# Kernel optimization log

Hardware: AMD Instinct MI355X
Metric: run time of the kernel (lower is better)

## Reference

```python
import jax, jax.numpy as jnp
import numpy as np

N, E, H, K, C, NMOD = 50000, 600000, 128, 5, 60, 12  # nodes, edges, hidden, hops, classes, 6 blocks * 2 modules


def setup_inputs() -> dict:
    key = jax.random.key(0)
    ks = iter(jax.random.split(key, 48))
    def rn(shape, scale=0.05):
        return jax.random.normal(next(ks), shape, jnp.float32) * scale
    return {
        "node_features": rn((N, 2), 1.0),
        "lap_pe": rn((N, K), 1.0),
        "edge_feat": rn((E, 4), 1.0),
        "src": jax.random.randint(next(ks), (E,), 0, N),
        "dst": jax.random.randint(next(ks), (E,), 0, N),
        "in_w": rn((2, H)), "in_b": jnp.zeros((H,), jnp.float32),
        "pos_w": rn((K, H)), "pos_b": jnp.zeros((H,), jnp.float32),
        "edge_w": rn((4, H)), "edge_b": jnp.zeros((H,), jnp.float32),
        "conv_w": rn((NMOD, 2, (K + 1) * H, H)), "conv_b": jnp.zeros((NMOD, 2, H), jnp.float32),
        "bn_g": jnp.ones((NMOD, 2, H), jnp.float32), "bn_b": jnp.zeros((NMOD, 2, H), jnp.float32),
        "ff_w": rn((NMOD, H, H)), "ff_b": jnp.zeros((NMOD, H), jnp.float32),
        "pose_w1": rn((H, H)), "pose_b1": jnp.zeros((H,), jnp.float32),
        "pose_w2": rn((H, 3)), "pose_b2": jnp.zeros((3,), jnp.float32),
        "lab_w1": rn((H, H)), "lab_b1": jnp.zeros((H,), jnp.float32),
        "lab_w2": rn((H, C)), "lab_b2": jnp.zeros((C,), jnp.float32),
    }


def _bn(x, g, b):
    # BatchNorm1d in training mode: stats over node axis
    m = x.mean(0)
    v = x.var(0)
    return (x - m) * jax.lax.rsqrt(v + 1e-5) * g + b


def reference(node_features, lap_pe, edge_feat, src, dst,
              in_w, in_b, pos_w, pos_b, edge_w, edge_b,
              conv_w, conv_b, bn_g, bn_b, ff_w, ff_b,
              pose_w1, pose_b1, pose_w2, pose_b2,
              lab_w1, lab_b1, lab_w2, lab_b2):
    seg = jax.ops.segment_sum
    # symmetric degree norm (in-degree, clamped to 1) as in DGL TAGConv
    deg = seg(jnp.ones((E,), node_features.dtype), dst, num_segments=N)
    norm = jnp.clip(deg, 1.0) ** -0.5  # [N]

    # edge feature aggregation: copy_e -> sum onto dst
    agg_e = seg(edge_feat @ edge_w + edge_b, dst, num_segments=N)  # [N,H]
    h = node_features @ in_w + in_b + lap_pe @ pos_w + pos_b + agg_e

    def tagconv(x, W, b):
        # fstack = [x, Ax, ..., A^K x] with A = D^-1/2 A D^-1/2, then single linear
        fs = [x]
        for _ in range(K):
            z = fs[-1] * norm[:, None]
            z = seg(z[src], dst, num_segments=N) * norm[:, None]
            fs.append(z)
        return jnp.concatenate(fs, axis=-1) @ W + b  # [N,H]

    for m in range(NMOD):  # 6 blocks x 2 TAGConvModules, sequential
        h_in = h
        h = jax.nn.relu(_bn(tagconv(h, conv_w[m, 0], conv_b[m, 0]), bn_g[m, 0], bn_b[m, 0]))
        h = jax.nn.relu(_bn(tagconv(h, conv_w[m, 1], conv_b[m, 1]), bn_g[m, 1], bn_b[m, 1]))
        h = h @ ff_w[m] + ff_b[m] + h_in  # dropout = identity (eval)

    pose = jax.nn.relu(h @ pose_w1 + pose_b1) @ pose_w2 + pose_b2  # [N,3]
    y = h.mean(0)  # dgl.mean_nodes (single batched graph)
    labels = jax.nn.relu(y @ lab_w1 + lab_b1) @ lab_w2 + lab_b2  # [C]
    return pose, labels
```

## Files before the change

kernel.cpp:

```cpp
#include <hip/hip_runtime.h>

#define NN 50000
#define EE 600000
#define HH 128
#define KK 5
#define CC 60
#define NMODS 12

typedef _Float16 f16;
typedef __attribute__((ext_vector_type(8))) _Float16 f16x8;
typedef __attribute__((ext_vector_type(4))) _Float16 f16x4;
typedef __attribute__((ext_vector_type(16))) float f32x16;

#define GLOBAL_AS __attribute__((address_space(1)))
#define LDS_AS __attribute__((address_space(3)))


__global__ void k_deg(const int* __restrict__ dst, int* __restrict__ deg) {
    int i = blockIdx.x * 256 + threadIdx.x;
    if (i < EE) atomicAdd(&deg[dst[i]], 1);
}

__global__ __launch_bounds__(1024) void k_scan(const int* __restrict__ deg, int* __restrict__ rs) {
    __shared__ int sm[1024];
    __shared__ int carry;
    int tid = threadIdx.x;
    if (tid == 0) carry = 0;
    __syncthreads();
    for (int base = 0; base < NN; base += 1024) {
        int i = base + tid;
        int v = (i < NN) ? deg[i] : 0;
        sm[tid] = v;
        __syncthreads();
        for (int off = 1; off < 1024; off <<= 1) {
            int t = (tid >= off) ? sm[tid - off] : 0;
            __syncthreads();
            sm[tid] += t;
            __syncthreads();
        }
        int incl = sm[tid];
        int c = carry;
        if (i < NN) rs[i] = c + incl - v;
        __syncthreads();
        if (tid == 1023) carry = c + incl;
        __syncthreads();
    }
    if (tid == 0) rs[NN] = carry;
}

__global__ void k_norm(const int* __restrict__ deg, float* __restrict__ norm) {
    int i = blockIdx.x * 256 + threadIdx.x;
    if (i < NN) {
        int d = deg[i];
        float fd = (float)(d < 1 ? 1 : d);
        norm[i] = 1.0f / sqrtf(fd);
    }
}

__global__ void k_fill(const int* __restrict__ src, const int* __restrict__ dst,
                       const int* __restrict__ rs, int* __restrict__ cursor,
                       int* __restrict__ csrc, int* __restrict__ ceid) {
    int i = blockIdx.x * 256 + threadIdx.x;
    if (i >= EE) return;
    int d = dst[i];
    int slot = atomicAdd(&cursor[d], 1);
    int p = rs[d] + slot;
    csrc[p] = src[i];
    ceid[p] = i;
}


__global__ void k_cvtw(const float* __restrict__ conv_w, const float* __restrict__ ff_w,
                       const float* __restrict__ pose_w1,
                       f16* __restrict__ wc, f16* __restrict__ wf, f16* __restrict__ wp) {
    int i = blockIdx.x * 256 + threadIdx.x;
    const int NCW = 24 * 128 * 768;
    const int NFW = 12 * 128 * 128;
    const int NPW = 128 * 128;
    if (i < NCW) {
        int mat = i / (128 * 768); int rem = i - mat * (128 * 768);
        int col = rem / 768; int k = rem - col * 768;
        wc[i] = (f16)conv_w[(size_t)mat * 768 * 128 + (size_t)k * 128 + col];
    } else if (i < NCW + NFW) {
        int j = i - NCW;
        int mat = j / (128 * 128); int rem = j - mat * (128 * 128);
        int col = rem / 128; int k = rem - col * 128;
        wf[j] = (f16)ff_w[(size_t)mat * 128 * 128 + k * 128 + col];
    } else if (i < NCW + NFW + NPW) {
        int j = i - NCW - NFW;
        int col = j / 128; int k = j - col * 128;
        wp[j] = (f16)pose_w1[k * 128 + col];
    }
}


__global__ __launch_bounds__(128) void k_h0(
    const float* __restrict__ nf, const float* __restrict__ pe, const float* __restrict__ ef,
    const int* __restrict__ rs, const int* __restrict__ ceid,
    const float* __restrict__ in_w, const float* __restrict__ in_b,
    const float* __restrict__ pos_w, const float* __restrict__ pos_b,
    const float* __restrict__ edge_w, const float* __restrict__ edge_b,
    float* __restrict__ h, f16* __restrict__ zc) {
    int n = blockIdx.x;
    int f = threadIdx.x;
    float v = in_b[f] + pos_b[f];
    v += nf[n * 2 + 0] * in_w[f] + nf[n * 2 + 1] * in_w[HH + f];
#pragma unroll
    for (int k = 0; k < KK; k++) v += pe[n * KK + k] * pos_w[k * HH + f];
    float e0 = edge_w[f], e1 = edge_w[HH + f], e2 = edge_w[2 * HH + f], e3 = edge_w[3 * HH + f];
    int s = rs[n], e = rs[n + 1];
    v += (float)(e - s) * edge_b[f];
    for (int i = s; i < e; i++) {
        int eid = ceid[i];
        float4 x = ((const float4*)ef)[eid];
        v += x.x * e0 + x.y * e1 + x.z * e2 + x.w * e3;
    }
    h[(size_t)n * HH + f] = v;
    zc[(size_t)n * 768 + f] = (f16)v;
}


__global__ __launch_bounds__(256) void k_prop16(
    const f16* __restrict__ zin, f16* __restrict__ zout,
    const float* __restrict__ norm, const int* __restrict__ rs,
    const int* __restrict__ csrc) {
    int tid = threadIdx.x;
    int n = blockIdx.x * 16 + (tid >> 4);
    int c = (tid & 15) * 8;
    int s = rs[n], e = rs[n + 1];
    float acc[8] = {0.f, 0.f, 0.f, 0.f, 0.f, 0.f, 0.f, 0.f};
    int i = s;
    for (; i + 1 < e; i += 2) {
        int s0 = csrc[i], s1 = csrc[i + 1];
        float w0 = norm[s0], w1 = norm[s1];
        f16x8 v0 = *(const f16x8*)(zin + (size_t)s0 * 768 + c);
        f16x8 v1 = *(const f16x8*)(zin + (size_t)s1 * 768 + c);
#pragma unroll
        for (int j = 0; j < 8; j++) acc[j] += (float)v0[j] * w0 + (float)v1[j] * w1;
    }
    if (i < e) {
        int s0 = csrc[i];
        float w0 = norm[s0];
        f16x8 v0 = *(const f16x8*)(zin + (size_t)s0 * 768 + c);
#pragma unroll
        for (int j = 0; j < 8; j++) acc[j] += (float)v0[j] * w0;
    }
    float nw = norm[n];
    f16x8 o;
#pragma unroll
    for (int j = 0; j < 8; j++) o[j] = (f16)(acc[j] * nw);
    *(f16x8*)(zout + (size_t)n * 768 + c) = o;
}


template <int KT, int BIAS, int RESID, int RELU, int WRZ>
__global__ __launch_bounds__(256) void k_mm(
    const f16* __restrict__ A, int lda, const f16* __restrict__ Wt,
    const float* __restrict__ bias, const float* __restrict__ Rsd,
    float* __restrict__ Y, f16* __restrict__ Zout) {
    __shared__ char smem[65536];
    char* As = smem;
    char* Bs = smem + 32768;
    int tid = threadIdx.x;
    int lane = tid & 63;
    int w = tid >> 6, wm = w >> 1, wn = w & 1;
    int n0 = blockIdx.x * 128;
    f32x16 acc[2][2] = {};
    for (int k0 = 0; k0 < KT; k0 += 128) {
        __syncthreads();
#pragma unroll
        for (int i = 0; i < 8; i++) {
            int p = (i * 256 + tid) * 16;
            int o = p ^ (((p >> 8) & 15) << 4);
            int r = o >> 8, ce = (o & 255) >> 1;
            int row = n0 + r; if (row >= NN) row = 0;
            const f16* ga = A + (size_t)row * lda + k0 + ce;
            char* lba = As + i * 4096 + w * 1024;
            __builtin_amdgcn_global_load_lds((const GLOBAL_AS void*)ga, (LDS_AS void*)lba, 16, 0, 0);
            const f16* gb = Wt + (size_t)r * KT + k0 + ce;
            char* lbb = Bs + i * 4096 + w * 1024;
            __builtin_amdgcn_global_load_lds((const GLOBAL_AS void*)gb, (LDS_AS void*)lbb, 16, 0, 0);
        }
        asm volatile("s_waitcnt vmcnt(0)" ::: "memory");
        __syncthreads();
#pragma unroll
        for (int s = 0; s < 8; s++) {
            int koff = s * 32 + (lane >> 5) * 16;
            f16x8 a[2], b[2];
#pragma unroll
            for (int m = 0; m < 2; m++) {
                int rl = wm * 64 + m * 32 + (lane & 31);
                int oa = (rl * 256 + koff) ^ ((rl & 15) << 4);
                a[m] = *(const f16x8*)(As + oa);
                int cl = wn * 64 + m * 32 + (lane & 31);
                int ob = (cl * 256 + koff) ^ ((cl & 15) << 4);
                b[m] = *(const f16x8*)(Bs + ob);
            }
#pragma unroll
            for (int m = 0; m < 2; m++)
#pragma unroll
                for (int nb = 0; nb < 2; nb++)
                    acc[m][nb] = __builtin_amdgcn_mfma_f32_32x32x16_f16(a[m], b[nb], acc[m][nb], 0, 0, 0);
        }
    }
#pragma unroll
    for (int m = 0; m < 2; m++) {
        int rb = n0 + wm * 64 + m * 32 + 4 * (lane >> 5);
#pragma unroll
        for (int nb = 0; nb < 2; nb++) {
            int col = wn * 64 + nb * 32 + (lane & 31);
            float bv = 0.f;
            if (BIAS) bv = bias[col];
#pragma unroll
            for (int r = 0; r < 16; r++) {
                int row = rb + (r & 3) + 8 * (r >> 2);
                if (row >= NN) continue;
                float v = acc[m][nb][r] + bv;
                if (RESID) v += Rsd[(size_t)row * HH + col];
                if (RELU) v = fmaxf(v, 0.f);
                Y[(size_t)row * HH + col] = v;
                if (WRZ) Zout[(size_t)row * 768 + col] = (f16)v;
            }
        }
    }
}


__global__ __launch_bounds__(256) void k_bnstats(const float* __restrict__ Y, float* __restrict__ part) {
    int tid = threadIdx.x;
    float s = 0.f, q = 0.f;
    for (int n = blockIdx.x * 2 + (tid >> 7); n < NN; n += 512) {
        float v = Y[(size_t)n * HH + (tid & 127)];
        s += v; q += v * v;
    }
    __shared__ float sh[512];
    sh[tid] = s; sh[256 + tid] = q;
    __syncthreads();
    if (tid < 128) {
        part[blockIdx.x * 256 + tid] = sh[tid] + sh[tid + 128];
        part[blockIdx.x * 256 + 128 + tid] = sh[256 + tid] + sh[256 + tid + 128];
    }
}

__global__ __launch_bounds__(128) void k_bnfin(const float* __restrict__ part,
                                               const float* __restrict__ g, const float* __restrict__ b,
                                               float* __restrict__ sc, float* __restrict__ sh) {
    int f = threadIdx.x;
    float s = 0.f, q = 0.f;
    for (int bi = 0; bi < 256; bi++) {
        s += part[bi * 256 + f];
        q += part[bi * 256 + 128 + f];
    }
    float mean = s / (float)NN;
    float var = q / (float)NN - mean * mean;
    float scale = g[f] / sqrtf(var + 1e-5f);
    sc[f] = scale;
    sh[f] = b[f] - mean * scale;
}

__global__ __launch_bounds__(256) void k_bnapply(const float* __restrict__ Y,
                                                 const float* __restrict__ sc, const float* __restrict__ sh,
                                                 float* __restrict__ H, f16* __restrict__ zc) {
    int idx = blockIdx.x * 256 + threadIdx.x;
    if (idx >= NN * 32) return;
    float4 v = ((const float4*)Y)[idx];
    int c = idx & 31;
    float4 a = ((const float4*)sc)[c];
    float4 b = ((const float4*)sh)[c];
    v.x = fmaxf(v.x * a.x + b.x, 0.f);
    v.y = fmaxf(v.y * a.y + b.y, 0.f);
    v.z = fmaxf(v.z * a.z + b.z, 0.f);
    v.w = fmaxf(v.w * a.w + b.w, 0.f);
    ((float4*)H)[idx] = v;
    int n = idx >> 5;
    f16x4 o;
    o[0] = (f16)v.x; o[1] = (f16)v.y; o[2] = (f16)v.z; o[3] = (f16)v.w;
    *(f16x4*)(zc + (size_t)n * 768 + c * 4) = o;
}


__global__ __launch_bounds__(128) void k_pose2(const float* __restrict__ T,
                                               const float* __restrict__ W2, const float* __restrict__ b2,
                                               float* __restrict__ out) {
    int tid = threadIdx.x;
    int n = blockIdx.x * 4 + (tid >> 5);
    int c = tid & 31;
    float4 tv = ((const float4*)T)[(size_t)n * 32 + c];
    float p0 = 0.f, p1 = 0.f, p2 = 0.f;
#pragma unroll
    for (int i = 0; i < 4; i++) {
        float t = (i == 0) ? tv.x : (i == 1) ? tv.y : (i == 2) ? tv.z : tv.w;
        int k = c * 4 + i;
        p0 += t * W2[k * 3 + 0];
        p1 += t * W2[k * 3 + 1];
        p2 += t * W2[k * 3 + 2];
    }
#pragma unroll
    for (int off = 16; off > 0; off >>= 1) {
        p0 += __shfl_down(p0, off, 32);
        p1 += __shfl_down(p1, off, 32);
        p2 += __shfl_down(p2, off, 32);
    }
    if (c == 0) {
        out[(size_t)n * 3 + 0] = p0 + b2[0];
        out[(size_t)n * 3 + 1] = p1 + b2[1];
        out[(size_t)n * 3 + 2] = p2 + b2[2];
    }
}

__global__ __launch_bounds__(256) void k_meanpart(const float* __restrict__ Y, float* __restrict__ part) {
    int tid = threadIdx.x;
    float s = 0.f;
    for (int n = blockIdx.x * 2 + (tid >> 7); n < NN; n += 512) {
        s += Y[(size_t)n * HH + (tid & 127)];
    }
    __shared__ float sh[256];
    sh[tid] = s;
    __syncthreads();
    if (tid < 128) part[blockIdx.x * 128 + tid] = sh[tid] + sh[tid + 128];
}

__global__ __launch_bounds__(128) void k_labels(const float* __restrict__ part,
                                                const float* __restrict__ w1, const float* __restrict__ b1,
                                                const float* __restrict__ w2, const float* __restrict__ b2,
                                                float* __restrict__ out) {
    __shared__ float ym[128];
    __shared__ float t2[128];
    int f = threadIdx.x;
    float s = 0.f;
    for (int bi = 0; bi < 256; bi++) s += part[bi * 128 + f];
    ym[f] = s / (float)NN;
    __syncthreads();
    float a = b1[f];
    for (int k = 0; k < 128; k++) a += ym[k] * w1[k * 128 + f];
    t2[f] = fmaxf(a, 0.f);
    __syncthreads();
    if (f < CC) {
        float a2 = b2[f];
        for (int k = 0; k < 128; k++) a2 += t2[k] * w2[k * CC + f];
        out[(size_t)NN * 3 + f] = a2;
    }
}


static inline size_t align256(size_t x) { return (x + 255) & ~(size_t)255; }

extern "C" void kernel_launch(void* const* d_in, const int* in_sizes, int n_in,
                              void* d_out, int out_size, void* d_ws, size_t ws_size,
                              hipStream_t stream) {
    const float* nf = (const float*)d_in[0];
    const float* pe = (const float*)d_in[1];
    const float* ef = (const float*)d_in[2];
    const int* src = (const int*)d_in[3];
    const int* dst = (const int*)d_in[4];
    const float* in_w = (const float*)d_in[5];
    const float* in_b = (const float*)d_in[6];
    const float* pos_w = (const float*)d_in[7];
    const float* pos_b = (const float*)d_in[8];
    const float* edge_w = (const float*)d_in[9];
    const float* edge_b = (const float*)d_in[10];
    const float* conv_w = (const float*)d_in[11];
    const float* bn_g = (const float*)d_in[13];
    const float* bn_b = (const float*)d_in[14];
    const float* ff_w = (const float*)d_in[15];
    const float* ff_b = (const float*)d_in[16];
    const float* pose_w1 = (const float*)d_in[17];
    const float* pose_b1 = (const float*)d_in[18];
    const float* pose_w2 = (const float*)d_in[19];
    const float* pose_b2 = (const float*)d_in[20];
    const float* lab_w1 = (const float*)d_in[21];
    const float* lab_b1 = (const float*)d_in[22];
    const float* lab_w2 = (const float*)d_in[23];
    const float* lab_b2 = (const float*)d_in[24];
    float* out = (float*)d_out;

    char* wsp = (char*)d_ws;
    size_t off = 0;
    auto alloc = [&](size_t bytes) -> void* {
        void* p = wsp + off;
        off += align256(bytes);
        return p;
    };
    float* norm = (float*)alloc((size_t)NN * 4);
    int* deg = (int*)alloc((size_t)NN * 4);
    int* rs = (int*)alloc((size_t)(NN + 1) * 4);
    int* cursor = (int*)alloc((size_t)NN * 4);
    int* csrc = (int*)alloc((size_t)EE * 4);
    int* ceid = (int*)alloc((size_t)EE * 4);
    float* hin = (float*)alloc((size_t)NN * HH * 4);
    float* hcur = (float*)alloc((size_t)NN * HH * 4);
    float* ybuf = (float*)alloc((size_t)NN * HH * 4);
    f16* zcat = (f16*)alloc((size_t)NN * 768 * 2);
    f16* wc = (f16*)alloc((size_t)24 * 128 * 768 * 2);
    f16* wf = (f16*)alloc((size_t)12 * 128 * 128 * 2);
    f16* wp = (f16*)alloc((size_t)128 * 128 * 2);
    float* part = (float*)alloc(256 * 256 * 4);
    float* mpart = (float*)alloc(256 * 128 * 4);
    float* bnsc = (float*)alloc(128 * 4);
    float* bnsh = (float*)alloc(128 * 4);
    (void)ws_size; (void)in_sizes; (void)n_in; (void)out_size;

    hipMemsetAsync(deg, 0, (size_t)NN * 4, stream);
    hipMemsetAsync(cursor, 0, (size_t)NN * 4, stream);
    int egrid = (EE + 255) / 256;
    k_deg<<<egrid, 256, 0, stream>>>(dst, deg);
    k_scan<<<1, 1024, 0, stream>>>(deg, rs);
    k_norm<<<(NN + 255) / 256, 256, 0, stream>>>(deg, norm);
    k_fill<<<egrid, 256, 0, stream>>>(src, dst, rs, cursor, csrc, ceid);

    const int NCVT = 24 * 128 * 768 + 12 * 128 * 128 + 128 * 128;
    k_cvtw<<<(NCVT + 255) / 256, 256, 0, stream>>>(conv_w, ff_w, pose_w1, wc, wf, wp);

    k_h0<<<NN, 128, 0, stream>>>(nf, pe, ef, rs, ceid, in_w, in_b, pos_w, pos_b, edge_w, edge_b,
                                 hin, zcat);

    const int mmgrid = (NN + 127) / 128;
    const int pgrid = NN / 16;
    const int agrid = (NN * 32) / 256;

    for (int m = 0; m < NMODS; m++) {
        for (int s = 0; s < 2; s++) {
            const f16* Wb = wc + (size_t)(m * 2 + s) * 128 * 768;
            for (int k = 1; k <= KK; k++) {
                k_prop16<<<pgrid, 256, 0, stream>>>(zcat + (k - 1) * 128, zcat + k * 128,
                                                    norm, rs, csrc);
            }
            k_mm<768, 0, 0, 0, 0><<<mmgrid, 256, 0, stream>>>(zcat, 768, Wb, nullptr, nullptr,
                                                              ybuf, nullptr);
            k_bnstats<<<256, 256, 0, stream>>>(ybuf, part);
            k_bnfin<<<1, 128, 0, stream>>>(part, bn_g + (size_t)(m * 2 + s) * HH,
                                           bn_b + (size_t)(m * 2 + s) * HH, bnsc, bnsh);
            k_bnapply<<<agrid, 256, 0, stream>>>(ybuf, bnsc, bnsh, hcur, zcat);
        }
        k_mm<128, 1, 1, 0, 1><<<mmgrid, 256, 0, stream>>>(zcat, 768, wf + (size_t)m * 128 * 128,
                                                          ff_b + (size_t)m * HH, hin, hin, zcat);
    }

    k_mm<128, 1, 0, 1, 0><<<mmgrid, 256, 0, stream>>>(zcat, 768, wp, pose_b1, nullptr,
                                                      ybuf, nullptr);
    k_pose2<<<NN / 4, 128, 0, stream>>>(ybuf, pose_w2, pose_b2, out);

    k_meanpart<<<256, 256, 0, stream>>>(hin, mpart);
    k_labels<<<1, 128, 0, stream>>>(mpart, lab_w1, lab_b1, lab_w2, lab_b2, out);
}
```

Baseline: 5.373 ms.

## Split hop features into planar slices, pad CSR rows, and degree-sort propagation

Stores each hop's features as a separate contiguous N×128 fp16 slice instead of interleaving them into 768-wide rows, so gathers touch denser rows. Each CSR row is padded to a multiple of four with zero-weight dummy edges, and per-edge norm weights are precomputed so propagation can load indices and weights as vectors. Nodes are bucketed by degree into a permutation so similar-work nodes share a wavefront, and the feature dimension is split across a second grid axis. The single-block scan becomes a three-kernel parallel scan, and the unused fp32 hcur write in bnapply is dropped. This adds preprocessing kernels and padded storage, and the padded dummy edges point at node 0 with zero weight.

Result: slower. 9.451 ms (+75.9%).

```diff
diff --git a/kernel.cpp b/kernel.cpp
--- a/kernel.cpp
+++ b/kernel.cpp
@@ -6,11 +6,19 @@
 #define KK 5
 #define CC 60
 #define NMODS 12
+#define MAXPE 750080
+#define SC_NB 49
+#define NB_PROP 782
+#define NCLS 32
 
 typedef _Float16 f16;
 typedef __attribute__((ext_vector_type(8))) _Float16 f16x8;
 typedef __attribute__((ext_vector_type(4))) _Float16 f16x4;
 typedef __attribute__((ext_vector_type(16))) float f32x16;
+typedef __attribute__((ext_vector_type(4))) int int4v;
+typedef __attribute__((ext_vector_type(4))) float f32x4;
+
+#define ZSL ((size_t)NN * 128)
 
 #define GLOBAL_AS __attribute__((address_space(1)))
 #define LDS_AS __attribute__((address_space(3)))
@@ -21,31 +29,56 @@
     if (i < EE) atomicAdd(&deg[dst[i]], 1);
 }
 
-__global__ __launch_bounds__(1024) void k_scan(const int* __restrict__ deg, int* __restrict__ rs) {
-    __shared__ int sm[1024];
-    __shared__ int carry;
-    int tid = threadIdx.x;
-    if (tid == 0) carry = 0;
+__global__ __launch_bounds__(256) void k_scan1(const int* __restrict__ deg,
+                                               int* __restrict__ rs, int* __restrict__ bsum) {
+    __shared__ int sm[256];
+    int t = threadIdx.x;
+    int base = blockIdx.x * 1024 + t * 4;
+    int d[4];
+#pragma unroll
+    for (int j = 0; j < 4; j++) {
+        int i = base + j;
+        d[j] = (i < NN) ? ((deg[i] + 3) & ~3) : 0;
+    }
+    int sum = d[0] + d[1] + d[2] + d[3];
+    sm[t] = sum;
     __syncthreads();
-    for (int base = 0; base < NN; base += 1024) {
-        int i = base + tid;
-        int v = (i < NN) ? deg[i] : 0;
-        sm[tid] = v;
+    for (int off = 1; off < 256; off <<= 1) {
+        int v = (t >= off) ? sm[t - off] : 0;
         __syncthreads();
-        for (int off = 1; off < 1024; off <<= 1) {
-            int t = (tid >= off) ? sm[tid - off] : 0;
-            __syncthreads();
-            sm[tid] += t;
-            __syncthreads();
-        }
-        int incl = sm[tid];
-        int c = carry;
-        if (i < NN) rs[i] = c + incl - v;
+        sm[t] += v;
         __syncthreads();
-        if (tid == 1023) carry = c + incl;
-        __syncthreads();
-    }
-    if (tid == 0) rs[NN] = carry;
+    }
+    int excl = sm[t] - sum;
+    int run = excl;
+#pragma unroll
+    for (int j = 0; j < 4; j++) {
+        int i = base + j;
+        if (i < NN) rs[i] = run;
+        run += d[j];
+    }
+    if (t == 255) bsum[blockIdx.x] = sm[t];
+}
+
+__global__ __launch_bounds__(64) void k_scan2(const int* __restrict__ bsum, int* __restrict__ binc) {
+    int l = threadIdx.x;
+    int v = (l < SC_NB) ? bsum[l] : 0;
+#pragma unroll
+    for (int off = 1; off < 64; off <<= 1) {
+        int tv = __shfl_up(v, off, 64);
+        if (l >= off) v += tv;
+    }
+    binc[l] = v;
+}
+
+__global__ __launch_bounds__(256) void k_scan3(const int* __restrict__ binc, int* __restrict__ rs) {
+    int i = blockIdx.x * 256 + threadIdx.x;
+    if (i < NN) {
+        int b = i >> 10;
+        if (b > 0) rs[i] += binc[b - 1];
+    } else if (i == NN) {
+        rs[NN] = binc[SC_NB - 1];
+    }
 }
 
 __global__ void k_norm(const int* __restrict__ deg, float* __restrict__ norm) {
@@ -58,15 +91,50 @@
 }
 
 __global__ void k_fill(const int* __restrict__ src, const int* __restrict__ dst,
-                       const int* __restrict__ rs, int* __restrict__ cursor,
-                       int* __restrict__ csrc, int* __restrict__ ceid) {
+                       const int* __restrict__ rs, const float* __restrict__ norm,
+                       int* __restrict__ cursor,
+                       int* __restrict__ csrc, float* __restrict__ ew, int* __restrict__ ceid) {
     int i = blockIdx.x * 256 + threadIdx.x;
     if (i >= EE) return;
     int d = dst[i];
     int slot = atomicAdd(&cursor[d], 1);
     int p = rs[d] + slot;
-    csrc[p] = src[i];
+    int s = src[i];
+    csrc[p] = s;
+    ew[p] = norm[s];
     ceid[p] = i;
+}
+
+__global__ void k_hist(const int* __restrict__ deg, int* __restrict__ chist) {
+    int i = blockIdx.x * 256 + threadIdx.x;
+    if (i < NN) {
+        int c = (deg[i] + 3) >> 2;
+        if (c > NCLS - 1) c = NCLS - 1;
+        atomicAdd(&chist[c], 1);
+    }
+}
+
+__global__ __launch_bounds__(64) void k_cscan(const int* __restrict__ chist, int* __restrict__ cbase) {
+    int l = threadIdx.x;
+    int own = (l < NCLS) ? chist[l] : 0;
+    int v = own;
+#pragma unroll
+    for (int off = 1; off < 64; off <<= 1) {
+        int tv = __shfl_up(v, off, 64);
+        if (l >= off) v += tv;
+    }
+    if (l < NCLS) cbase[l] = v - own;
+}
+
+__global__ void k_permf(const int* __restrict__ deg, const int* __restrict__ cbase,
+                        int* __restrict__ ccur, int* __restrict__ perm) {
+    int i = blockIdx.x * 256 + threadIdx.x;
+    if (i < NN) {
+        int c = (deg[i] + 3) >> 2;
+        if (c > NCLS - 1) c = NCLS - 1;
+        int slot = atomicAdd(&ccur[c], 1);
+        perm[cbase[c] + slot] = i;
+    }
 }
 
 
@@ -96,7 +164,8 @@
 
 __global__ __launch_bounds__(128) void k_h0(
     const float* __restrict__ nf, const float* __restrict__ pe, const float* __restrict__ ef,
-    const int* __restrict__ rs, const int* __restrict__ ceid,
+    const int* __restrict__ rs, const int* __restrict__ ceid, const float* __restrict__ ew,
+    const int* __restrict__ deg,
     const float* __restrict__ in_w, const float* __restrict__ in_b,
     const float* __restrict__ pos_w, const float* __restrict__ pos_b,
     const float* __restrict__ edge_w, const float* __restrict__ edge_b,
@@ -109,53 +178,54 @@
     for (int k = 0; k < KK; k++) v += pe[n * KK + k] * pos_w[k * HH + f];
     float e0 = edge_w[f], e1 = edge_w[HH + f], e2 = edge_w[2 * HH + f], e3 = edge_w[3 * HH + f];
     int s = rs[n], e = rs[n + 1];
-    v += (float)(e - s) * edge_b[f];
+    v += (float)deg[n] * edge_b[f];
     for (int i = s; i < e; i++) {
+        if (ew[i] == 0.f) continue;
         int eid = ceid[i];
         float4 x = ((const float4*)ef)[eid];
         v += x.x * e0 + x.y * e1 + x.z * e2 + x.w * e3;
     }
     h[(size_t)n * HH + f] = v;
-    zc[(size_t)n * 768 + f] = (f16)v;
+    zc[(size_t)n * 128 + f] = (f16)v;
 }
 
 
 __global__ __launch_bounds__(256) void k_prop16(
     const f16* __restrict__ zin, f16* __restrict__ zout,
     const float* __restrict__ norm, const int* __restrict__ rs,
-    const int* __restrict__ csrc) {
+    const int* __restrict__ csrc, const float* __restrict__ ew,
+    const int* __restrict__ perm) {
     int tid = threadIdx.x;
-    int n = blockIdx.x * 16 + (tid >> 4);
-    int c = (tid & 15) * 8;
+    int idx = blockIdx.x * 64 + (tid >> 2);
+    if (idx >= NN) return;
+    int n = perm[idx];
+    int c = blockIdx.y * 32 + (tid & 3) * 8;
     int s = rs[n], e = rs[n + 1];
+    const f16* zp = zin + c;
     float acc[8] = {0.f, 0.f, 0.f, 0.f, 0.f, 0.f, 0.f, 0.f};
-    int i = s;
-    for (; i + 1 < e; i += 2) {
-        int s0 = csrc[i], s1 = csrc[i + 1];
-        float w0 = norm[s0], w1 = norm[s1];
-        f16x8 v0 = *(const f16x8*)(zin + (size_t)s0 * 768 + c);
-        f16x8 v1 = *(const f16x8*)(zin + (size_t)s1 * 768 + c);
-#pragma unroll
-        for (int j = 0; j < 8; j++) acc[j] += (float)v0[j] * w0 + (float)v1[j] * w1;
-    }
-    if (i < e) {
-        int s0 = csrc[i];
-        float w0 = norm[s0];
-        f16x8 v0 = *(const f16x8*)(zin + (size_t)s0 * 768 + c);
-#pragma unroll
-        for (int j = 0; j < 8; j++) acc[j] += (float)v0[j] * w0;
+    for (int i = s; i < e; i += 4) {
+        int4v id4 = __builtin_nontemporal_load((const int4v*)(csrc + i));
+        f32x4 w4 = __builtin_nontemporal_load((const f32x4*)(ew + i));
+        f16x8 v0 = *(const f16x8*)(zp + (size_t)id4.x * 128);
+        f16x8 v1 = *(const f16x8*)(zp + (size_t)id4.y * 128);
+        f16x8 v2 = *(const f16x8*)(zp + (size_t)id4.z * 128);
+        f16x8 v3 = *(const f16x8*)(zp + (size_t)id4.w * 128);
+#pragma unroll
+        for (int j = 0; j < 8; j++)
+            acc[j] += (float)v0[j] * w4.x + (float)v1[j] * w4.y +
+                      (float)v2[j] * w4.z + (float)v3[j] * w4.w;
     }
     float nw = norm[n];
     f16x8 o;
 #pragma unroll
     for (int j = 0; j < 8; j++) o[j] = (f16)(acc[j] * nw);
-    *(f16x8*)(zout + (size_t)n * 768 + c) = o;
+    *(f16x8*)(zout + (size_t)n * 128 + c) = o;
 }
 
 
 template <int KT, int BIAS, int RESID, int RELU, int WRZ>
 __global__ __launch_bounds__(256) void k_mm(
-    const f16* __restrict__ A, int lda, const f16* __restrict__ Wt,
+    const f16* __restrict__ A, const f16* __restrict__ Wt,
     const float* __restrict__ bias, const float* __restrict__ Rsd,
     float* __restrict__ Y, f16* __restrict__ Zout) {
     __shared__ char smem[65536];
@@ -168,13 +238,14 @@
     f32x16 acc[2][2] = {};
     for (int k0 = 0; k0 < KT; k0 += 128) {
         __syncthreads();
+        const f16* Asl = A + (size_t)(k0 >> 7) * ZSL;
 #pragma unroll
         for (int i = 0; i < 8; i++) {
             int p = (i * 256 + tid) * 16;
             int o = p ^ (((p >> 8) & 15) << 4);
             int r = o >> 8, ce = (o & 255) >> 1;
             int row = n0 + r; if (row >= NN) row = 0;
-            const f16* ga = A + (size_t)row * lda + k0 + ce;
+            const f16* ga = Asl + (size_t)row * 128 + ce;
             char* lba = As + i * 4096 + w * 1024;
             __builtin_amdgcn_global_load_lds((const GLOBAL_AS void*)ga, (LDS_AS void*)lba, 16, 0, 0);
             const f16* gb = Wt + (size_t)r * KT + k0 + ce;
@@ -219,7 +290,7 @@
                 if (RESID) v += Rsd[(size_t)row * HH + col];
                 if (RELU) v = fmaxf(v, 0.f);
                 Y[(size_t)row * HH + col] = v;
-                if (WRZ) Zout[(size_t)row * 768 + col] = (f16)v;
+                if (WRZ) Zout[(size_t)row * 128 + col] = (f16)v;
             }
         }
     }
@@ -260,22 +331,20 @@
 
 __global__ __launch_bounds__(256) void k_bnapply(const float* __restrict__ Y,
                                                  const float* __restrict__ sc, const float* __restrict__ sh,
-                                                 float* __restrict__ H, f16* __restrict__ zc) {
+                                                 f16* __restrict__ zc) {
     int idx = blockIdx.x * 256 + threadIdx.x;
     if (idx >= NN * 32) return;
     float4 v = ((const float4*)Y)[idx];
     int c = idx & 31;
     float4 a = ((const float4*)sc)[c];
     float4 b = ((const float4*)sh)[c];
-    v.x = fmaxf(v.x * a.x + b.x, 0.f);
-    v.y = fmaxf(v.y * a.y + b.y, 0.f);
-    v.z = fmaxf(v.z * a.z + b.z, 0.f);
-    v.w = fmaxf(v.w * a.w + b.w, 0.f);
-    ((float4*)H)[idx] = v;
     int n = idx >> 5;
     f16x4 o;
-    o[0] = (f16)v.x; o[1] = (f16)v.y; o[2] = (f16)v.z; o[3] = (f16)v.w;
-    *(f16x4*)(zc + (size_t)n * 768 + c * 4) = o;
+    o[0] = (f16)fmaxf(v.x * a.x + b.x, 0.f);
+    o[1] = (f16)fmaxf(v.y * a.y + b.y, 0.f);
+    o[2] = (f16)fmaxf(v.z * a.z + b.z, 0.f);
+    o[3] = (f16)fmaxf(v.w * a.w + b.w, 0.f);
+    *(f16x4*)(zc + (size_t)n * 128 + c * 4) = o;
 }
 
 
@@ -385,12 +454,18 @@
     int* deg = (int*)alloc((size_t)NN * 4);
     int* rs = (int*)alloc((size_t)(NN + 1) * 4);
     int* cursor = (int*)alloc((size_t)NN * 4);
-    int* csrc = (int*)alloc((size_t)EE * 4);
-    int* ceid = (int*)alloc((size_t)EE * 4);
+    int* csrc = (int*)alloc((size_t)MAXPE * 4);
+    float* ew = (float*)alloc((size_t)MAXPE * 4);
+    int* ceid = (int*)alloc((size_t)MAXPE * 4);
+    int* bsum = (int*)alloc(64 * 4);
+    int* binc = (int*)alloc(64 * 4);
+    int* chist = (int*)alloc(NCLS * 4);
+    int* cbase = (int*)alloc(NCLS * 4);
+    int* ccur = (int*)alloc(NCLS * 4);
+    int* perm = (int*)alloc((size_t)NN * 4);
     float* hin = (float*)alloc((size_t)NN * HH * 4);
-    float* hcur = (float*)alloc((size_t)NN * HH * 4);
     float* ybuf = (float*)alloc((size_t)NN * HH * 4);
-    f16* zcat = (f16*)alloc((size_t)NN * 768 * 2);
+    f16* zcat = (f16*)alloc((size_t)6 * ZSL * 2);
     f16* wc = (f16*)alloc((size_t)24 * 128 * 768 * 2);
     f16* wf = (f16*)alloc((size_t)12 * 128 * 128 * 2);
     f16* wp = (f16*)alloc((size_t)128 * 128 * 2);
@@ -402,42 +477,51 @@
 
     hipMemsetAsync(deg, 0, (size_t)NN * 4, stream);
     hipMemsetAsync(cursor, 0, (size_t)NN * 4, stream);
+    hipMemsetAsync(csrc, 0, (size_t)MAXPE * 4, stream);
+    hipMemsetAsync(ew, 0, (size_t)MAXPE * 4, stream);
+    hipMemsetAsync(chist, 0, NCLS * 4, stream);
+    hipMemsetAsync(ccur, 0, NCLS * 4, stream);
     int egrid = (EE + 255) / 256;
     k_deg<<<egrid, 256, 0, stream>>>(dst, deg);
-    k_scan<<<1, 1024, 0, stream>>>(deg, rs);
+    k_scan1<<<SC_NB, 256, 0, stream>>>(deg, rs, bsum);
+    k_scan2<<<1, 64, 0, stream>>>(bsum, binc);
+    k_scan3<<<(NN + 256) / 256, 256, 0, stream>>>(binc, rs);
     k_norm<<<(NN + 255) / 256, 256, 0, stream>>>(deg, norm);
-    k_fill<<<egrid, 256, 0, stream>>>(src, dst, rs, cursor, csrc, ceid);
+    k_fill<<<egrid, 256, 0, stream>>>(src, dst, rs, norm, cursor, csrc, ew, ceid);
+    k_hist<<<(NN + 255) / 256, 256, 0, stream>>>(deg, chist);
+    k_cscan<<<1, 64, 0, stream>>>(chist, cbase);
+    k_permf<<<(NN + 255) / 256, 256, 0, stream>>>(deg, cbase, ccur, perm);
 
     const int NCVT = 24 * 128 * 768 + 12 * 128 * 128 + 128 * 128;
     k_cvtw<<<(NCVT + 255) / 256, 256, 0, stream>>>(conv_w, ff_w, pose_w1, wc, wf, wp);
 
-    k_h0<<<NN, 128, 0, stream>>>(nf, pe, ef, rs, ceid, in_w, in_b, pos_w, pos_b, edge_w, edge_b,
-                                 hin, zcat);
+    k_h0<<<NN, 128, 0, stream>>>(nf, pe, ef, rs, ceid, ew, deg, in_w, in_b, pos_w, pos_b,
+                                 edge_w, edge_b, hin, zcat);
 
     const int mmgrid = (NN + 127) / 128;
-    const int pgrid = NN / 16;
+    const dim3 pgrid(NB_PROP, 4);
     const int agrid = (NN * 32) / 256;
 
     for (int m = 0; m < NMODS; m++) {
         for (int s = 0; s < 2; s++) {
             const f16* Wb = wc + (size_t)(m * 2 + s) * 128 * 768;
             for (int k = 1; k <= KK; k++) {
-                k_prop16<<<pgrid, 256, 0, stream>>>(zcat + (k - 1) * 128, zcat + k * 128,
-                                                    norm, rs, csrc);
+                k_prop16<<<pgrid, 256, 0, stream>>>(zcat + (size_t)(k - 1) * ZSL,
+                                                    zcat + (size_t)k * ZSL,
+                                                    norm, rs, csrc, ew, perm);
             }
-            k_mm<768, 0, 0, 0, 0><<<mmgrid, 256, 0, stream>>>(zcat, 768, Wb, nullptr, nullptr,
+            k_mm<768, 0, 0, 0, 0><<<mmgrid, 256, 0, stream>>>(zcat, Wb, nullptr, nullptr,
                                                               ybuf, nullptr);
             k_bnstats<<<256, 256, 0, stream>>>(ybuf, part);
             k_bnfin<<<1, 128, 0, stream>>>(part, bn_g + (size_t)(m * 2 + s) * HH,
                                            bn_b + (size_t)(m * 2 + s) * HH, bnsc, bnsh);
-            k_bnapply<<<agrid, 256, 0, stream>>>(ybuf, bnsc, bnsh, hcur, zcat);
+            k_bnapply<<<agrid, 256, 0, stream>>>(ybuf, bnsc, bnsh, zcat);
         }
-        k_mm<128, 1, 1, 0, 1><<<mmgrid, 256, 0, stream>>>(zcat, 768, wf + (size_t)m * 128 * 128,
+        k_mm<128, 1, 1, 0, 1><<<mmgrid, 256, 0, stream>>>(zcat, wf + (size_t)m * 128 * 128,
                                                           ff_b + (size_t)m * HH, hin, hin, zcat);
     }
 
-    k_mm<128, 1, 0, 1, 0><<<mmgrid, 256, 0, stream>>>(zcat, 768, wp, pose_b1, nullptr,
-                                                      ybuf, nullptr);
+    k_mm<128, 1, 0, 1, 0><<<mmgrid, 256, 0, stream>>>(zcat, wp, pose_b1, nullptr, ybuf, nullptr);
     k_pose2<<<NN / 4, 128, 0, stream>>>(ybuf, pose_w2, pose_b2, out);
 
     k_meanpart<<<256, 256, 0, stream>>>(hin, mpart);
```
